# Kernel optimization log

Measured on AMD Instinct MI355X. Metric: run time of the kernel, lower is better.

Reference implementation:

```python
import jax, jax.numpy as jnp
import numpy as np

BATCH, IN, OUT, P = 8192, 1024, 1024, 8

def setup_inputs() -> dict:
    key = jax.random.key(0)
    k1, k2, k3 = jax.random.split(key, 3)
    x = jax.random.normal(k1, (BATCH, IN), dtype=jnp.float32)
    # per-(output,input) basis coefficients, init ~ randn*0.1 as in torch module
    coefficients = jax.random.normal(k2, (OUT, IN, P), dtype=jnp.float32) * 0.1
    weights = jax.random.normal(k3, (OUT, IN), dtype=jnp.float32)
    return {"x": x, "coefficients": coefficients, "weights": weights}

def reference(x, coefficients, weights):
    # out[b,o] = sum_i x[b,i] * (sum_p coef[o,i,p]) * weights[o,i]
    # == x @ (coef_sum * weights)^T  -- single fused GEMM
    w_eff = coefficients.sum(axis=-1) * weights  # [O, I]
    return jnp.einsum('bi,oi->bo', x, w_eff)
```

## Files before the change

### kernel.cpp

```cpp
#include <hip/hip_runtime.h>
#include <hip/hip_bf16.h>
#include <stdint.h>

#define BATCH 8192
#define IN    1024
#define OUTD  1024
#define PBASIS 8

typedef __attribute__((ext_vector_type(8))) short bf16x8;
typedef __attribute__((ext_vector_type(4))) float floatx4;

__device__ __forceinline__ unsigned short f2bf(float f) {
    union { float f; unsigned u; } v; v.f = f;
    unsigned u = v.u;
    u += 0x7fffu + ((u >> 16) & 1u);
    return (unsigned short)(u >> 16);
}

__global__ void prep_kernel(const float* __restrict__ x,
                            const float* __restrict__ coef,
                            const float* __restrict__ w,
                            unsigned short* __restrict__ xb,
                            unsigned short* __restrict__ weff) {
    int b = blockIdx.x;
    int tid = threadIdx.x;
    if (b < 4096) {
        int idx = b * 256 + tid;
        const float4* p = (const float4*)(x + (size_t)idx * 8);
        float4 a = p[0], c = p[1];
        uint4 o;
        o.x = (unsigned)f2bf(a.x) | ((unsigned)f2bf(a.y) << 16);
        o.y = (unsigned)f2bf(a.z) | ((unsigned)f2bf(a.w) << 16);
        o.z = (unsigned)f2bf(c.x) | ((unsigned)f2bf(c.y) << 16);
        o.w = (unsigned)f2bf(c.z) | ((unsigned)f2bf(c.w) << 16);
        ((uint4*)xb)[idx] = o;
    } else {
        int idx = (b - 4096) * 256 + tid;
        size_t e0 = (size_t)idx * 2;
        const float4* c4 = (const float4*)(coef + e0 * PBASIS);
        float4 a = c4[0], bb = c4[1], c = c4[2], d = c4[3];
        float s0 = (a.x + a.y + a.z + a.w) + (bb.x + bb.y + bb.z + bb.w);
        float s1 = (c.x + c.y + c.z + c.w) + (d.x + d.y + d.z + d.w);
        float2 ww = ((const float2*)w)[idx];
        unsigned b0 = f2bf(s0 * ww.x);
        unsigned b1 = f2bf(s1 * ww.y);
        ((unsigned*)weff)[idx] = b0 | (b1 << 16);
    }
}

__device__ __forceinline__ void gload_lds16(const void* g, void* l) {
    __builtin_amdgcn_global_load_lds(
        (const __attribute__((address_space(1))) unsigned int*)g,
        (__attribute__((address_space(3))) unsigned int*)l,
        16, 0, 0);
}

#define BARRIER()  asm volatile("s_barrier" ::: "memory")
#define WAIT_V6L0() asm volatile("s_waitcnt vmcnt(6) lgkmcnt(0)" ::: "memory")
#define WAIT_V0L0() asm volatile("s_waitcnt vmcnt(0) lgkmcnt(0)" ::: "memory")

__global__ __launch_bounds__(512, 2) void gemm_bt(
        const unsigned short* __restrict__ A,
        const unsigned short* __restrict__ B,
        float* __restrict__ C) {
    constexpr int K = IN, BK = 64, NT = K / BK;
    constexpr int STG = 49152;
    constexpr int ES = 132;
    __shared__ __align__(16) char smem[3 * STG];
    float* ebuf = (float*)smem;

    const int tid  = threadIdx.x;
    const int bm   = blockIdx.x, bn = blockIdx.y;
    const int lane = tid & 63;
    const int wave = tid >> 6;
    const int wm   = wave >> 1;
    const int wn   = wave & 1;
    const int t    = lane & 15;
    const int q    = lane >> 4;
    const int r8   = t & 7;

    int g0 = tid,        ra0 = g0 >> 3, ca0 = (g0 & 7) ^ (ra0 & 7);
    int g1 = 512 + tid,  ra1 = g1 >> 3, ca1 = (g1 & 7) ^ (ra1 & 7);
    int g2 = 1024 + tid, ra2 = g2 >> 3, ca2 = (g2 & 7) ^ (ra2 & 7);
    int g3 = 1536 + tid, ra3 = g3 >> 3, ca3 = (g3 & 7) ^ (ra3 & 7);
    int h0 = tid,        rb0 = h0 >> 3, cb0 = (h0 & 7) ^ (rb0 & 7);
    int h1 = 512 + tid,  rb1 = h1 >> 3, cb1 = (h1 & 7) ^ (rb1 & 7);

    const unsigned short* gA0 = A + (size_t)(bm * 256 + ra0) * K + ca0 * 8;
    const unsigned short* gA1 = A + (size_t)(bm * 256 + ra1) * K + ca1 * 8;
    const unsigned short* gA2 = A + (size_t)(bm * 256 + ra2) * K + ca2 * 8;
    const unsigned short* gA3 = A + (size_t)(bm * 256 + ra3) * K + ca3 * 8;
    const unsigned short* gB0 = B + (size_t)(bn * 128 + rb0) * K + cb0 * 8;
    const unsigned short* gB1 = B + (size_t)(bn * 128 + rb1) * K + cb1 * 8;

    const int dA0 = g0 * 16, dA1 = g1 * 16, dA2 = g2 * 16, dA3 = g3 * 16;
    const int dB0 = 32768 + h0 * 16, dB1 = 32768 + h1 * 16;

    const int aO0 = ((wm * 64 + t) * 64 + ((0 + q) ^ r8) * 8) * 2;
    const int aO1 = ((wm * 64 + t) * 64 + ((4 + q) ^ r8) * 8) * 2;
    const int bO0 = 32768 + ((wn * 64 + t) * 64 + ((0 + q) ^ r8) * 8) * 2;
    const int bO1 = 32768 + ((wn * 64 + t) * 64 + ((4 + q) ^ r8) * 8) * 2;

    floatx4 acc[4][4];
#pragma unroll
    for (int i = 0; i < 4; ++i)
#pragma unroll
        for (int j = 0; j < 4; ++j)
            acc[i][j] = (floatx4){0.f, 0.f, 0.f, 0.f};

#define STAGE_A3(sp, ko)                                            \
    {                                                               \
        gload_lds16(gA0 + (ko), (sp) + dA0);                        \
        gload_lds16(gA1 + (ko), (sp) + dA1);                        \
        gload_lds16(gA2 + (ko), (sp) + dA2);                        \
    }
#define STAGE_B3(sp, ko)                                            \
    {                                                               \
        gload_lds16(gA3 + (ko), (sp) + dA3);                        \
        gload_lds16(gB0 + (ko), (sp) + dB0);                        \
        gload_lds16(gB1 + (ko), (sp) + dB1);                        \
    }
#define PHASE(sb, aO, bO)                                           \
    {                                                               \
        const char* ab = (sb) + (aO);                               \
        const char* bb = (sb) + (bO);                               \
        bf16x8 af0 = *(const bf16x8*)(ab + 0 * 2048);               \
        bf16x8 af1 = *(const bf16x8*)(ab + 1 * 2048);               \
        bf16x8 af2 = *(const bf16x8*)(ab + 2 * 2048);               \
        bf16x8 af3 = *(const bf16x8*)(ab + 3 * 2048);               \
        bf16x8 bf0 = *(const bf16x8*)(bb + 0 * 2048);               \
        bf16x8 bf1 = *(const bf16x8*)(bb + 1 * 2048);               \
        bf16x8 bf2 = *(const bf16x8*)(bb + 2 * 2048);               \
        bf16x8 bf3 = *(const bf16x8*)(bb + 3 * 2048);               \
        bf16x8 afv[4] = {af0, af1, af2, af3};                       \
        bf16x8 bfv[4] = {bf0, bf1, bf2, bf3};                       \
        __builtin_amdgcn_s_setprio(1);                              \
        _Pragma("unroll")                                           \
        for (int i = 0; i < 4; ++i)                                 \
            _Pragma("unroll")                                       \
            for (int j = 0; j < 4; ++j)                             \
                acc[i][j] = __builtin_amdgcn_mfma_f32_16x16x32_bf16(\
                    afv[i], bfv[j], acc[i][j], 0, 0, 0);            \
        __builtin_amdgcn_s_setprio(0);                              \
    }

    {
        char* s0 = smem;
        char* s1 = smem + STG;
        STAGE_A3(s0, 0); STAGE_B3(s0, 0);
        STAGE_A3(s1, BK); STAGE_B3(s1, BK);
        WAIT_V6L0();
        BARRIER();
    }

    int cur = 0;
    for (int kt = 0; kt < NT; ++kt) {
        char* sb = smem + cur * STG;
        int nx = cur + 2; if (nx >= 3) nx -= 3;
        char* sp = smem + nx * STG;
        const int kpre = (kt + 2) * BK;
        const bool pre = (kt < NT - 2);

        if (pre) STAGE_A3(sp, kpre);
        PHASE(sb, aO0, bO0);
        if (pre) STAGE_B3(sp, kpre);
        PHASE(sb, aO1, bO1);

        if (pre) { WAIT_V6L0(); }
        else     { WAIT_V0L0(); }
        BARRIER();
        ++cur; if (cur == 3) cur = 0;
    }
#undef PHASE
#undef STAGE_A3
#undef STAGE_B3

    __syncthreads();

#pragma unroll
    for (int tm = 0; tm < 4; ++tm)
#pragma unroll
        for (int tn = 0; tn < 4; ++tn)
#pragma unroll
            for (int r = 0; r < 4; ++r)
                ebuf[(wm * 64 + tm * 16 + q * 4 + r) * ES
                     + wn * 64 + tn * 16 + t] = acc[tm][tn][r];
    __syncthreads();
#pragma unroll
    for (int ps = 0; ps < 16; ++ps) {
        int row  = ps * 16 + (tid >> 5);
        int col4 = tid & 31;
        float4 v = *(const float4*)(ebuf + row * ES + col4 * 4);
        *(float4*)(C + (size_t)(bm * 256 + row) * OUTD + bn * 128 + col4 * 4) = v;
    }
}

extern "C" void kernel_launch(void* const* d_in, const int* in_sizes, int n_in,
                              void* d_out, int out_size, void* d_ws, size_t ws_size,
                              hipStream_t stream) {
    const float* x    = (const float*)d_in[0];
    const float* coef = (const float*)d_in[1];
    const float* w    = (const float*)d_in[2];
    float* out = (float*)d_out;

    unsigned short* xb   = (unsigned short*)d_ws;
    unsigned short* weff = (unsigned short*)((char*)d_ws + (size_t)BATCH * IN * 2);

    prep_kernel<<<6144, 256, 0, stream>>>(x, coef, w, xb, weff);
    gemm_bt<<<dim3(BATCH / 256, OUTD / 128), 512, 0, stream>>>(xb, weff, out);
}
```

Measured before the change: 122.5 us.

## Load GEMM B operand directly into registers, staging only A through LDS

Each wave now reads its B (weight) MFMA fragments straight from global memory into registers, double-buffered across K-steps. Only the A tile still goes through the three-stage LDS ring, which shrinks each stage to 32 KB. The goal is to cut LDS traffic and LDS reads for B and to shorten the staging critical path. In exchange, B is fetched redundantly by the four waves sharing a column, which leans on the caches, and holding two sets of B fragments in registers adds about 64 VGPRs under a 512x2 launch bound, so spills are possible.

```diff
diff --git a/kernel.cpp b/kernel.cpp
--- a/kernel.cpp
+++ b/kernel.cpp
@@ -15,6 +15,10 @@
     unsigned u = v.u;
     u += 0x7fffu + ((u >> 16) & 1u);
     return (unsigned short)(u >> 16);
+}
+
+__device__ __forceinline__ bf16x8 u4bf(uint4 v) {
+    union { uint4 u; bf16x8 b; } x; x.u = v; return x.b;
 }
 
 __global__ void prep_kernel(const float* __restrict__ x,
@@ -56,17 +60,17 @@
 }
 
 #define BARRIER()  asm volatile("s_barrier" ::: "memory")
-#define WAIT_V6L0() asm volatile("s_waitcnt vmcnt(6) lgkmcnt(0)" ::: "memory")
-#define WAIT_V0L0() asm volatile("s_waitcnt vmcnt(0) lgkmcnt(0)" ::: "memory")
+#define WAIT_V4()  asm volatile("s_waitcnt vmcnt(4) lgkmcnt(0)" ::: "memory")
+#define WAIT_V0()  asm volatile("s_waitcnt vmcnt(0) lgkmcnt(0)" ::: "memory")
 
 __global__ __launch_bounds__(512, 2) void gemm_bt(
         const unsigned short* __restrict__ A,
         const unsigned short* __restrict__ B,
         float* __restrict__ C) {
     constexpr int K = IN, BK = 64, NT = K / BK;
-    constexpr int STG = 49152;
+    constexpr int ASTG = 32768;
     constexpr int ES = 132;
-    __shared__ __align__(16) char smem[3 * STG];
+    __shared__ __align__(16) char smem[135168];
     float* ebuf = (float*)smem;
 
     const int tid  = threadIdx.x;
@@ -79,27 +83,25 @@
     const int q    = lane >> 4;
     const int r8   = t & 7;
 
-    int g0 = tid,        ra0 = g0 >> 3, ca0 = (g0 & 7) ^ (ra0 & 7);
-    int g1 = 512 + tid,  ra1 = g1 >> 3, ca1 = (g1 & 7) ^ (ra1 & 7);
-    int g2 = 1024 + tid, ra2 = g2 >> 3, ca2 = (g2 & 7) ^ (ra2 & 7);
-    int g3 = 1536 + tid, ra3 = g3 >> 3, ca3 = (g3 & 7) ^ (ra3 & 7);
-    int h0 = tid,        rb0 = h0 >> 3, cb0 = (h0 & 7) ^ (rb0 & 7);
-    int h1 = 512 + tid,  rb1 = h1 >> 3, cb1 = (h1 & 7) ^ (rb1 & 7);
+    int g0 = tid,         ra0 = g0 >> 3, ca0 = (g0 & 7) ^ (ra0 & 7);
+    int g1 = 512 + tid,   ra1 = g1 >> 3, ca1 = (g1 & 7) ^ (ra1 & 7);
+    int g2 = 1024 + tid,  ra2 = g2 >> 3, ca2 = (g2 & 7) ^ (ra2 & 7);
+    int g3 = 1536 + tid,  ra3 = g3 >> 3, ca3 = (g3 & 7) ^ (ra3 & 7);
 
     const unsigned short* gA0 = A + (size_t)(bm * 256 + ra0) * K + ca0 * 8;
     const unsigned short* gA1 = A + (size_t)(bm * 256 + ra1) * K + ca1 * 8;
     const unsigned short* gA2 = A + (size_t)(bm * 256 + ra2) * K + ca2 * 8;
     const unsigned short* gA3 = A + (size_t)(bm * 256 + ra3) * K + ca3 * 8;
-    const unsigned short* gB0 = B + (size_t)(bn * 128 + rb0) * K + cb0 * 8;
-    const unsigned short* gB1 = B + (size_t)(bn * 128 + rb1) * K + cb1 * 8;
 
     const int dA0 = g0 * 16, dA1 = g1 * 16, dA2 = g2 * 16, dA3 = g3 * 16;
-    const int dB0 = 32768 + h0 * 16, dB1 = 32768 + h1 * 16;
 
     const int aO0 = ((wm * 64 + t) * 64 + ((0 + q) ^ r8) * 8) * 2;
     const int aO1 = ((wm * 64 + t) * 64 + ((4 + q) ^ r8) * 8) * 2;
-    const int bO0 = 32768 + ((wn * 64 + t) * 64 + ((0 + q) ^ r8) * 8) * 2;
-    const int bO1 = 32768 + ((wn * 64 + t) * 64 + ((4 + q) ^ r8) * 8) * 2;
+
+    const unsigned short* gBt0 = B + (size_t)(bn * 128 + wn * 64 + 0 * 16 + t) * K + q * 8;
+    const unsigned short* gBt1 = B + (size_t)(bn * 128 + wn * 64 + 1 * 16 + t) * K + q * 8;
+    const unsigned short* gBt2 = B + (size_t)(bn * 128 + wn * 64 + 2 * 16 + t) * K + q * 8;
+    const unsigned short* gBt3 = B + (size_t)(bn * 128 + wn * 64 + 3 * 16 + t) * K + q * 8;
 
     floatx4 acc[4][4];
 #pragma unroll
@@ -108,72 +110,97 @@
         for (int j = 0; j < 4; ++j)
             acc[i][j] = (floatx4){0.f, 0.f, 0.f, 0.f};
 
-#define STAGE_A3(sp, ko)                                            \
+#define STAGE_A(sp, ko)                                             \
     {                                                               \
         gload_lds16(gA0 + (ko), (sp) + dA0);                        \
         gload_lds16(gA1 + (ko), (sp) + dA1);                        \
         gload_lds16(gA2 + (ko), (sp) + dA2);                        \
-    }
-#define STAGE_B3(sp, ko)                                            \
+        gload_lds16(gA3 + (ko), (sp) + dA3);                        \
+    }
+#define LOADB(kt, d00, d01, d10, d11, d20, d21, d30, d31)           \
     {                                                               \
-        gload_lds16(gA3 + (ko), (sp) + dA3);                        \
-        gload_lds16(gB0 + (ko), (sp) + dB0);                        \
-        gload_lds16(gB1 + (ko), (sp) + dB1);                        \
-    }
-#define PHASE(sb, aO, bO)                                           \
+        d00 = *(const uint4*)(gBt0 + (kt) * 64);                    \
+        d01 = *(const uint4*)(gBt0 + (kt) * 64 + 32);               \
+        d10 = *(const uint4*)(gBt1 + (kt) * 64);                    \
+        d11 = *(const uint4*)(gBt1 + (kt) * 64 + 32);               \
+        d20 = *(const uint4*)(gBt2 + (kt) * 64);                    \
+        d21 = *(const uint4*)(gBt2 + (kt) * 64 + 32);               \
+        d30 = *(const uint4*)(gBt3 + (kt) * 64);                    \
+        d31 = *(const uint4*)(gBt3 + (kt) * 64 + 32);               \
+    }
+#define PHASE(sb, aOff, B0, B1, B2, B3)                             \
     {                                                               \
-        const char* ab = (sb) + (aO);                               \
-        const char* bb = (sb) + (bO);                               \
-        bf16x8 af0 = *(const bf16x8*)(ab + 0 * 2048);               \
-        bf16x8 af1 = *(const bf16x8*)(ab + 1 * 2048);               \
-        bf16x8 af2 = *(const bf16x8*)(ab + 2 * 2048);               \
-        bf16x8 af3 = *(const bf16x8*)(ab + 3 * 2048);               \
-        bf16x8 bf0 = *(const bf16x8*)(bb + 0 * 2048);               \
-        bf16x8 bf1 = *(const bf16x8*)(bb + 1 * 2048);               \
-        bf16x8 bf2 = *(const bf16x8*)(bb + 2 * 2048);               \
-        bf16x8 bf3 = *(const bf16x8*)(bb + 3 * 2048);               \
-        bf16x8 afv[4] = {af0, af1, af2, af3};                       \
-        bf16x8 bfv[4] = {bf0, bf1, bf2, bf3};                       \
+        const char* ab = (const char*)(sb) + (aOff);                \
+        bf16x8 a0 = *(const bf16x8*)(ab + 0 * 2048);                \
+        bf16x8 a1 = *(const bf16x8*)(ab + 1 * 2048);                \
+        bf16x8 a2 = *(const bf16x8*)(ab + 2 * 2048);                \
+        bf16x8 a3 = *(const bf16x8*)(ab + 3 * 2048);                \
+        bf16x8 av[4] = {a0, a1, a2, a3};                            \
+        bf16x8 bv[4] = {u4bf(B0), u4bf(B1), u4bf(B2), u4bf(B3)};    \
         __builtin_amdgcn_s_setprio(1);                              \
         _Pragma("unroll")                                           \
         for (int i = 0; i < 4; ++i)                                 \
             _Pragma("unroll")                                       \
             for (int j = 0; j < 4; ++j)                             \
                 acc[i][j] = __builtin_amdgcn_mfma_f32_16x16x32_bf16(\
-                    afv[i], bfv[j], acc[i][j], 0, 0, 0);            \
+                    av[i], bv[j], acc[i][j], 0, 0, 0);              \
         __builtin_amdgcn_s_setprio(0);                              \
     }
 
+    uint4 cb00, cb01, cb10, cb11, cb20, cb21, cb30, cb31;
+    uint4 nb00, nb01, nb10, nb11, nb20, nb21, nb30, nb31;
+
+    STAGE_A(smem, 0);
+    STAGE_A(smem + ASTG, BK);
+    LOADB(0, cb00, cb01, cb10, cb11, cb20, cb21, cb30, cb31);
+    WAIT_V0();
+    BARRIER();
+
+    int c = 0;
+    for (int it = 0; it < 7; ++it) {
+        const int kt0 = 2 * it, kt1 = 2 * it + 1;
+        {
+            char* sb = smem + c * ASTG;
+            int s2 = c + 2; if (s2 >= 3) s2 -= 3;
+            LOADB(kt0 + 1, nb00, nb01, nb10, nb11, nb20, nb21, nb30, nb31);
+            STAGE_A(smem + s2 * ASTG, (kt0 + 2) * BK);
+            PHASE(sb, aO0, cb00, cb10, cb20, cb30);
+            PHASE(sb, aO1, cb01, cb11, cb21, cb31);
+            WAIT_V4();
+            BARRIER();
+            ++c; if (c >= 3) c -= 3;
+        }
+        {
+            char* sb = smem + c * ASTG;
+            int s2 = c + 2; if (s2 >= 3) s2 -= 3;
+            LOADB(kt1 + 1, cb00, cb01, cb10, cb11, cb20, cb21, cb30, cb31);
+            STAGE_A(smem + s2 * ASTG, (kt1 + 2) * BK);
+            PHASE(sb, aO0, nb00, nb10, nb20, nb30);
+            PHASE(sb, aO1, nb01, nb11, nb21, nb31);
+            WAIT_V4();
+            BARRIER();
+            ++c; if (c >= 3) c -= 3;
+        }
+    }
     {
-        char* s0 = smem;
-        char* s1 = smem + STG;
-        STAGE_A3(s0, 0); STAGE_B3(s0, 0);
-        STAGE_A3(s1, BK); STAGE_B3(s1, BK);
-        WAIT_V6L0();
+        char* sb = smem + c * ASTG;
+        LOADB(15, nb00, nb01, nb10, nb11, nb20, nb21, nb30, nb31);
+        PHASE(sb, aO0, cb00, cb10, cb20, cb30);
+        PHASE(sb, aO1, cb01, cb11, cb21, cb31);
+        WAIT_V0();
         BARRIER();
-    }
-
-    int cur = 0;
-    for (int kt = 0; kt < NT; ++kt) {
-        char* sb = smem + cur * STG;
-        int nx = cur + 2; if (nx >= 3) nx -= 3;
-        char* sp = smem + nx * STG;
-        const int kpre = (kt + 2) * BK;
-        const bool pre = (kt < NT - 2);
-
-        if (pre) STAGE_A3(sp, kpre);
-        PHASE(sb, aO0, bO0);
-        if (pre) STAGE_B3(sp, kpre);
-        PHASE(sb, aO1, bO1);
-
-        if (pre) { WAIT_V6L0(); }
-        else     { WAIT_V0L0(); }
+        ++c; if (c >= 3) c -= 3;
+    }
+    {
+        char* sb = smem + c * ASTG;
+        PHASE(sb, aO0, nb00, nb10, nb20, nb30);
+        PHASE(sb, aO1, nb01, nb11, nb21, nb31);
+        WAIT_V0();
         BARRIER();
-        ++cur; if (cur == 3) cur = 0;
     }
 #undef PHASE
-#undef STAGE_A3
-#undef STAGE_B3
+#undef LOADB
+#undef STAGE_A
 
     __syncthreads();
 
```

Result: slower. 148.5 us (+21.2%).

## Fuse x fp32-to-bf16 conversion into GEMM A-tile loading via registers

Applied to the files above, without the earlier changes.

Drops the separate pass that converts x to bf16 in workspace. The GEMM now reads fp32 x straight into registers one stage ahead, converts it with packed cvt instructions and writes it into swizzled LDS, while B still goes through direct global-to-LDS loads. This removes a full write and re-read of a bf16 copy of x. In exchange the GEMM reads twice as many A bytes per tile, each thread holds many more registers for the in-flight float4s, and the pipeline is more complex with two register sets and unrolled K iterations.

```diff
diff --git a/kernel.cpp b/kernel.cpp
--- a/kernel.cpp
+++ b/kernel.cpp
@@ -17,35 +17,25 @@
     return (unsigned short)(u >> 16);
 }
 
-__global__ void prep_kernel(const float* __restrict__ x,
-                            const float* __restrict__ coef,
+__device__ __forceinline__ unsigned cvtpk(float lo, float hi) {
+    unsigned r;
+    asm("v_cvt_pk_bf16_f32 %0, %1, %2" : "=v"(r) : "v"(lo), "v"(hi));
+    return r;
+}
+
+__global__ void prep_kernel(const float* __restrict__ coef,
                             const float* __restrict__ w,
-                            unsigned short* __restrict__ xb,
                             unsigned short* __restrict__ weff) {
-    int b = blockIdx.x;
-    int tid = threadIdx.x;
-    if (b < 4096) {
-        int idx = b * 256 + tid;
-        const float4* p = (const float4*)(x + (size_t)idx * 8);
-        float4 a = p[0], c = p[1];
-        uint4 o;
-        o.x = (unsigned)f2bf(a.x) | ((unsigned)f2bf(a.y) << 16);
-        o.y = (unsigned)f2bf(a.z) | ((unsigned)f2bf(a.w) << 16);
-        o.z = (unsigned)f2bf(c.x) | ((unsigned)f2bf(c.y) << 16);
-        o.w = (unsigned)f2bf(c.z) | ((unsigned)f2bf(c.w) << 16);
-        ((uint4*)xb)[idx] = o;
-    } else {
-        int idx = (b - 4096) * 256 + tid;
-        size_t e0 = (size_t)idx * 2;
-        const float4* c4 = (const float4*)(coef + e0 * PBASIS);
-        float4 a = c4[0], bb = c4[1], c = c4[2], d = c4[3];
-        float s0 = (a.x + a.y + a.z + a.w) + (bb.x + bb.y + bb.z + bb.w);
-        float s1 = (c.x + c.y + c.z + c.w) + (d.x + d.y + d.z + d.w);
-        float2 ww = ((const float2*)w)[idx];
-        unsigned b0 = f2bf(s0 * ww.x);
-        unsigned b1 = f2bf(s1 * ww.y);
-        ((unsigned*)weff)[idx] = b0 | (b1 << 16);
-    }
+    int idx = blockIdx.x * 256 + threadIdx.x;
+    size_t e0 = (size_t)idx * 2;
+    const float4* c4 = (const float4*)(coef + e0 * PBASIS);
+    float4 a = c4[0], bb = c4[1], c = c4[2], d = c4[3];
+    float s0 = (a.x + a.y + a.z + a.w) + (bb.x + bb.y + bb.z + bb.w);
+    float s1 = (c.x + c.y + c.z + c.w) + (d.x + d.y + d.z + d.w);
+    float2 ww = ((const float2*)w)[idx];
+    unsigned b0 = f2bf(s0 * ww.x);
+    unsigned b1 = f2bf(s1 * ww.y);
+    ((unsigned*)weff)[idx] = b0 | (b1 << 16);
 }
 
 __device__ __forceinline__ void gload_lds16(const void* g, void* l) {
@@ -55,12 +45,12 @@
         16, 0, 0);
 }
 
-#define BARRIER()  asm volatile("s_barrier" ::: "memory")
-#define WAIT_V6L0() asm volatile("s_waitcnt vmcnt(6) lgkmcnt(0)" ::: "memory")
-#define WAIT_V0L0() asm volatile("s_waitcnt vmcnt(0) lgkmcnt(0)" ::: "memory")
+#define BARRIER()    asm volatile("s_barrier" ::: "memory")
+#define WAIT_V10L0() asm volatile("s_waitcnt vmcnt(10) lgkmcnt(0)" ::: "memory")
+#define WAIT_V0L0()  asm volatile("s_waitcnt vmcnt(0) lgkmcnt(0)" ::: "memory")
 
 __global__ __launch_bounds__(512, 2) void gemm_bt(
-        const unsigned short* __restrict__ A,
+        const float* __restrict__ X,
         const unsigned short* __restrict__ B,
         float* __restrict__ C) {
     constexpr int K = IN, BK = 64, NT = K / BK;
@@ -79,17 +69,17 @@
     const int q    = lane >> 4;
     const int r8   = t & 7;
 
-    int g0 = tid,        ra0 = g0 >> 3, ca0 = (g0 & 7) ^ (ra0 & 7);
-    int g1 = 512 + tid,  ra1 = g1 >> 3, ca1 = (g1 & 7) ^ (ra1 & 7);
-    int g2 = 1024 + tid, ra2 = g2 >> 3, ca2 = (g2 & 7) ^ (ra2 & 7);
-    int g3 = 1536 + tid, ra3 = g3 >> 3, ca3 = (g3 & 7) ^ (ra3 & 7);
-    int h0 = tid,        rb0 = h0 >> 3, cb0 = (h0 & 7) ^ (rb0 & 7);
-    int h1 = 512 + tid,  rb1 = h1 >> 3, cb1 = (h1 & 7) ^ (rb1 & 7);
-
-    const unsigned short* gA0 = A + (size_t)(bm * 256 + ra0) * K + ca0 * 8;
-    const unsigned short* gA1 = A + (size_t)(bm * 256 + ra1) * K + ca1 * 8;
-    const unsigned short* gA2 = A + (size_t)(bm * 256 + ra2) * K + ca2 * 8;
-    const unsigned short* gA3 = A + (size_t)(bm * 256 + ra3) * K + ca3 * 8;
+    int g0 = tid,         ra0 = g0 >> 3, ca0 = (g0 & 7) ^ (ra0 & 7);
+    int g1 = 512 + tid,   ra1 = g1 >> 3, ca1 = (g1 & 7) ^ (ra1 & 7);
+    int g2 = 1024 + tid,  ra2 = g2 >> 3, ca2 = (g2 & 7) ^ (ra2 & 7);
+    int g3 = 1536 + tid,  ra3 = g3 >> 3, ca3 = (g3 & 7) ^ (ra3 & 7);
+    int h0 = tid,         rb0 = h0 >> 3, cb0 = (h0 & 7) ^ (rb0 & 7);
+    int h1 = 512 + tid,   rb1 = h1 >> 3, cb1 = (h1 & 7) ^ (rb1 & 7);
+
+    const float* gx0 = X + (size_t)(bm * 256 + ra0) * K + ca0 * 8;
+    const float* gx1 = X + (size_t)(bm * 256 + ra1) * K + ca1 * 8;
+    const float* gx2 = X + (size_t)(bm * 256 + ra2) * K + ca2 * 8;
+    const float* gx3 = X + (size_t)(bm * 256 + ra3) * K + ca3 * 8;
     const unsigned short* gB0 = B + (size_t)(bn * 128 + rb0) * K + cb0 * 8;
     const unsigned short* gB1 = B + (size_t)(bn * 128 + rb1) * K + cb1 * 8;
 
@@ -108,22 +98,42 @@
         for (int j = 0; j < 4; ++j)
             acc[i][j] = (floatx4){0.f, 0.f, 0.f, 0.f};
 
-#define STAGE_A3(sp, ko)                                            \
-    {                                                               \
-        gload_lds16(gA0 + (ko), (sp) + dA0);                        \
-        gload_lds16(gA1 + (ko), (sp) + dA1);                        \
-        gload_lds16(gA2 + (ko), (sp) + dA2);                        \
-    }
-#define STAGE_B3(sp, ko)                                            \
-    {                                                               \
-        gload_lds16(gA3 + (ko), (sp) + dA3);                        \
+#define ISSUE_A(d0,d1,d2,d3,d4,d5,d6,d7, kf)                        \
+    {                                                               \
+        d0 = *(const float4*)(gx0 + (kf));                          \
+        d1 = *(const float4*)(gx0 + (kf) + 4);                      \
+        d2 = *(const float4*)(gx1 + (kf));                          \
+        d3 = *(const float4*)(gx1 + (kf) + 4);                      \
+        d4 = *(const float4*)(gx2 + (kf));                          \
+        d5 = *(const float4*)(gx2 + (kf) + 4);                      \
+        d6 = *(const float4*)(gx3 + (kf));                          \
+        d7 = *(const float4*)(gx3 + (kf) + 4);                      \
+    }
+#define STAGE_B(sp, ko)                                             \
+    {                                                               \
         gload_lds16(gB0 + (ko), (sp) + dB0);                        \
         gload_lds16(gB1 + (ko), (sp) + dB1);                        \
     }
+#define CVT_WRITE(sw, s0,s1,s2,s3,s4,s5,s6,s7)                      \
+    {                                                               \
+        uint4 v;                                                    \
+        v.x = cvtpk(s0.x, s0.y); v.y = cvtpk(s0.z, s0.w);           \
+        v.z = cvtpk(s1.x, s1.y); v.w = cvtpk(s1.z, s1.w);           \
+        *(uint4*)((sw) + dA0) = v;                                  \
+        v.x = cvtpk(s2.x, s2.y); v.y = cvtpk(s2.z, s2.w);           \
+        v.z = cvtpk(s3.x, s3.y); v.w = cvtpk(s3.z, s3.w);           \
+        *(uint4*)((sw) + dA1) = v;                                  \
+        v.x = cvtpk(s4.x, s4.y); v.y = cvtpk(s4.z, s4.w);           \
+        v.z = cvtpk(s5.x, s5.y); v.w = cvtpk(s5.z, s5.w);           \
+        *(uint4*)((sw) + dA2) = v;                                  \
+        v.x = cvtpk(s6.x, s6.y); v.y = cvtpk(s6.z, s6.w);           \
+        v.z = cvtpk(s7.x, s7.y); v.w = cvtpk(s7.z, s7.w);           \
+        *(uint4*)((sw) + dA3) = v;                                  \
+    }
 #define PHASE(sb, aO, bO)                                           \
     {                                                               \
-        const char* ab = (sb) + (aO);                               \
-        const char* bb = (sb) + (bO);                               \
+        const char* ab = (const char*)(sb) + (aO);                  \
+        const char* bb = (const char*)(sb) + (bO);                  \
         bf16x8 af0 = *(const bf16x8*)(ab + 0 * 2048);               \
         bf16x8 af1 = *(const bf16x8*)(ab + 1 * 2048);               \
         bf16x8 af2 = *(const bf16x8*)(ab + 2 * 2048);               \
@@ -144,36 +154,66 @@
         __builtin_amdgcn_s_setprio(0);                              \
     }
 
+    float4 pa0, pa1, pa2, pa3, pa4, pa5, pa6, pa7;
+    float4 na0, na1, na2, na3, na4, na5, na6, na7;
+
+    ISSUE_A(na0,na1,na2,na3,na4,na5,na6,na7, 0);
+    STAGE_B(smem, 0);
+    ISSUE_A(pa0,pa1,pa2,pa3,pa4,pa5,pa6,pa7, 64);
+    STAGE_B(smem + STG, BK);
+    CVT_WRITE(smem, na0,na1,na2,na3,na4,na5,na6,na7);
+    WAIT_V10L0();
+    BARRIER();
+
+    int cur = 0;
+    for (int it = 0; it < 7; ++it) {
+        const int kt0 = 2 * it, kt1 = kt0 + 1;
+        {
+            char* sb = smem + cur * STG;
+            int w1 = cur + 1; if (w1 >= 3) w1 -= 3;
+            int p2 = cur + 2; if (p2 >= 3) p2 -= 3;
+            ISSUE_A(na0,na1,na2,na3,na4,na5,na6,na7, (kt0 + 2) * 64);
+            STAGE_B(smem + p2 * STG, (kt0 + 2) * BK);
+            CVT_WRITE(smem + w1 * STG, pa0,pa1,pa2,pa3,pa4,pa5,pa6,pa7);
+            PHASE(sb, aO0, bO0);
+            PHASE(sb, aO1, bO1);
+            WAIT_V10L0();
+            BARRIER();
+            cur = w1;
+        }
+        {
+            char* sb = smem + cur * STG;
+            int w1 = cur + 1; if (w1 >= 3) w1 -= 3;
+            int p2 = cur + 2; if (p2 >= 3) p2 -= 3;
+            ISSUE_A(pa0,pa1,pa2,pa3,pa4,pa5,pa6,pa7, (kt1 + 2) * 64);
+            STAGE_B(smem + p2 * STG, (kt1 + 2) * BK);
+            CVT_WRITE(smem + w1 * STG, na0,na1,na2,na3,na4,na5,na6,na7);
+            PHASE(sb, aO0, bO0);
+            PHASE(sb, aO1, bO1);
+            WAIT_V10L0();
+            BARRIER();
+            cur = w1;
+        }
+    }
     {
-        char* s0 = smem;
-        char* s1 = smem + STG;
-        STAGE_A3(s0, 0); STAGE_B3(s0, 0);
-        STAGE_A3(s1, BK); STAGE_B3(s1, BK);
-        WAIT_V6L0();
+        char* sb = smem + cur * STG;
+        int w1 = cur + 1; if (w1 >= 3) w1 -= 3;
+        CVT_WRITE(smem + w1 * STG, pa0,pa1,pa2,pa3,pa4,pa5,pa6,pa7);
+        PHASE(sb, aO0, bO0);
+        PHASE(sb, aO1, bO1);
+        WAIT_V0L0();
         BARRIER();
-    }
-
-    int cur = 0;
-    for (int kt = 0; kt < NT; ++kt) {
+        cur = w1;
+    }
+    {
         char* sb = smem + cur * STG;
-        int nx = cur + 2; if (nx >= 3) nx -= 3;
-        char* sp = smem + nx * STG;
-        const int kpre = (kt + 2) * BK;
-        const bool pre = (kt < NT - 2);
-
-        if (pre) STAGE_A3(sp, kpre);
         PHASE(sb, aO0, bO0);
-        if (pre) STAGE_B3(sp, kpre);
         PHASE(sb, aO1, bO1);
-
-        if (pre) { WAIT_V6L0(); }
-        else     { WAIT_V0L0(); }
-        BARRIER();
-        ++cur; if (cur == 3) cur = 0;
     }
 #undef PHASE
-#undef STAGE_A3
-#undef STAGE_B3
+#undef CVT_WRITE
+#undef STAGE_B
+#undef ISSUE_A
 
     __syncthreads();
 
@@ -203,9 +243,8 @@
     const float* w    = (const float*)d_in[2];
     float* out = (float*)d_out;
 
-    unsigned short* xb   = (unsigned short*)d_ws;
-    unsigned short* weff = (unsigned short*)((char*)d_ws + (size_t)BATCH * IN * 2);
-
-    prep_kernel<<<6144, 256, 0, stream>>>(x, coef, w, xb, weff);
-    gemm_bt<<<dim3(BATCH / 256, OUTD / 128), 512, 0, stream>>>(xb, weff, out);
-}
+    unsigned short* weff = (unsigned short*)d_ws;
+
+    prep_kernel<<<2048, 256, 0, stream>>>(coef, w, weff);
+    gemm_bt<<<dim3(BATCH / 256, OUTD / 128), 512, 0, stream>>>(x, weff, out);
+}
```

Measured after the change: 139.4 us. +13.8%, slower.
